# Kernel optimization log

Measured on AMD Instinct MI355X. Metric: run time of the kernel, lower is better.

Reference implementation:

```python
import jax, jax.numpy as jnp
import numpy as np

B, S, D, NH = 2, 2048, 2048, 16
HD = D // NH  # 128


def setup_inputs() -> dict:
    key = jax.random.key(0)
    ks = jax.random.split(key, 7)
    s = 1.0 / np.sqrt(D)
    return {
        "hidden_states": jax.random.normal(ks[0], (B, S, D), dtype=jnp.float32),
        "Wq": jax.random.normal(ks[1], (D, D), dtype=jnp.float32) * s,
        "Wk": jax.random.normal(ks[2], (D, D), dtype=jnp.float32) * s,
        "Wv": jax.random.normal(ks[3], (D, D), dtype=jnp.float32) * s,
        "Wo": jax.random.normal(ks[4], (D, D), dtype=jnp.float32) * s,
        # phase projections: hidden -> num_heads (zero-init in the module; use small
        # random values so the phase path is numerically exercised)
        "Wpq": jax.random.normal(ks[5], (D, NH), dtype=jnp.float32) * 0.02,
        "Wpk": jax.random.normal(ks[6], (D, NH), dtype=jnp.float32) * 0.02,
    }


def reference(hidden_states, Wq, Wk, Wv, Wo, Wpq, Wpk):
    x = hidden_states  # [B,S,D]
    # ---- base_attn: standard causal multi-head self-attention ----
    q = (x @ Wq).reshape(B, S, NH, HD).transpose(0, 2, 1, 3)  # [B,H,S,hd]
    k = (x @ Wk).reshape(B, S, NH, HD).transpose(0, 2, 1, 3)
    v = (x @ Wv).reshape(B, S, NH, HD).transpose(0, 2, 1, 3)
    scores = jnp.einsum("bhqd,bhkd->bhqk", q, k) / np.sqrt(HD)  # [B,H,S,S]
    causal = jnp.tril(jnp.ones((S, S), dtype=bool))
    scores = jnp.where(causal, scores, jnp.float32(-1e9))
    probs = jax.nn.softmax(scores, axis=-1)
    ctx = jnp.einsum("bhqk,bhkd->bhqd", probs, v)  # [B,H,S,hd]
    attn_output = ctx.transpose(0, 2, 1, 3).reshape(B, S, D) @ Wo  # [B,S,D]
    # ---- phase modulation ----
    # original: cos(pq[b,q,None,h] - pk[b,None,k,h]).mean(dims=(k,h))  -> [B,S]
    # identity: cos(a-b) = cos a * cos b + sin a * sin b lets us avoid the
    # [B,S,S,H] tensor; the math is identical.
    pq = x @ Wpq  # [B,S,H]
    pk = x @ Wpk  # [B,S,H]
    Ck = jnp.cos(pk).sum(axis=1)  # [B,H]
    Sk = jnp.sin(pk).sum(axis=1)  # [B,H]
    phase_mod = (jnp.cos(pq) * Ck[:, None, :] + jnp.sin(pq) * Sk[:, None, :]).sum(-1) / (S * NH)  # [B,S]
    return attn_output * (1.0 + 0.1 * phase_mod[..., None])
```

## Files before the change

### kernel.cpp

```cpp
#include <hip/hip_runtime.h>
#include <hip/hip_bf16.h>

typedef __attribute__((ext_vector_type(8))) short short8;
typedef __attribute__((ext_vector_type(4))) float f32x4;
typedef __attribute__((ext_vector_type(16))) float f32x16;
typedef __attribute__((ext_vector_type(4))) int i32x4;
typedef unsigned short u16;

#define S_LEN 2048
#define D_DIM 2048
#define NHEAD 16
#define HDIM 128
#define M_ROWS 4096

#define MFMA(a,b,c) __builtin_amdgcn_mfma_f32_16x16x32_bf16(a,b,c,0,0,0)
#define MFMA32(a,b,c) __builtin_amdgcn_mfma_f32_32x32x16_bf16(a,b,c,0,0,0)

__device__ __forceinline__ u16 f2bf(float f) {
  union { float f; unsigned u; } v; v.f = f;
  unsigned r = v.u + 0x7fffu + ((v.u >> 16) & 1u);
  return (u16)(r >> 16);
}

__device__ __forceinline__ void async16(void* lds, const void* g) {
  __builtin_amdgcn_global_load_lds(
      (const __attribute__((address_space(1))) unsigned*)g,
      (__attribute__((address_space(3))) unsigned*)lds, 16, 0, 0);
}

__device__ __forceinline__ unsigned cvtpk(float lo, float hi) {
  unsigned r;
  asm("v_cvt_pk_bf16_f32 %0, %1, %2" : "=v"(r) : "v"(lo), "v"(hi));
  return r;
}
__device__ __forceinline__ void plswap(unsigned& x, unsigned& y) {
  asm("v_permlane32_swap_b32 %0, %1" : "+v"(x), "+v"(y));
}

__global__ __launch_bounds__(256) void k_prep(const float* __restrict__ W0,
                                              const float* __restrict__ W1,
                                              const float* __restrict__ W2,
                                              const float* __restrict__ W3,
                                              u16* __restrict__ T0, u16* __restrict__ T1,
                                              u16* __restrict__ T2, u16* __restrict__ T3,
                                              const float* __restrict__ x,
                                              u16* __restrict__ xb) {
  const int z = blockIdx.z;
  if (z < 4) {
    __shared__ u16 tile[32][33];
    const float* W = (z == 0) ? W0 : (z == 1) ? W1 : (z == 2) ? W2 : W3;
    u16* Wt = (z == 0) ? T0 : (z == 1) ? T1 : (z == 2) ? T2 : T3;
    int n0 = blockIdx.x * 32, k0 = blockIdx.y * 32;
    int tx = threadIdx.x & 31, ty = threadIdx.x >> 5;
#pragma unroll
    for (int i = 0; i < 4; i++)
      tile[ty + i * 8][tx] = f2bf(W[(size_t)(k0 + ty + i * 8) * D_DIM + n0 + tx]);
    __syncthreads();
#pragma unroll
    for (int i = 0; i < 4; i++)
      Wt[(size_t)(n0 + ty + i * 8) * D_DIM + k0 + tx] = tile[tx][ty + i * 8];
  } else {
    const int row0 = (z - 4) * 2048 + blockIdx.y * 32;
    const int col0 = blockIdx.x * 32;
    const int r = threadIdx.x >> 3, c4 = threadIdx.x & 7;
    const float4 v = *reinterpret_cast<const float4*>(
        &x[(size_t)(row0 + r) * D_DIM + col0 + c4 * 4]);
    ushort4 o;
    o.x = f2bf(v.x); o.y = f2bf(v.y); o.z = f2bf(v.z); o.w = f2bf(v.w);
    *reinterpret_cast<ushort4*>(&xb[(size_t)(row0 + r) * D_DIM + col0 + c4 * 4]) = o;
  }
}

template <int MODE>
__device__ __forceinline__ void gemm_body(const u16* __restrict__ A,
                                          const u16* __restrict__ Bt,
                                          void* __restrict__ outp,
                                          u16* __restrict__ Vt,
                                          const float* __restrict__ fac,
                                          char* lds) {
  constexpr int BUFSZ = 49152;
  const int m0 = blockIdx.y * 128, n0 = blockIdx.x * 256;
  const int t = threadIdx.x;
  const int w = t >> 6, l = t & 63;
  const int wr = (w >> 2) * 64, wc = (w & 3) * 64;
  const int lr = l & 15, lq = l >> 4;
  const char* Ab = (const char*)A;
  const char* Bb = (const char*)Bt;

  f32x4 acc[4][4] = {};

  const int sub = w >> 2, ww = w & 3;
  const int abase = (ww & 1) * 16 + (ww >> 1) * 64;
  const int bbase = (w >> 1) * 64 + (w & 1) * 16;
  const int rr = l >> 2, sl = l & 3;

  auto stageA = [&](int tt, int nb, int mh) {
    const int base = abase + mh * 32;
    const int row = base + rr;
    async16(lds + nb * BUFSZ + sub * 8192 + base * 64,
            Ab + (size_t)(m0 + row) * 4096 + tt * 128 + sub * 64 +
                ((sl ^ ((row >> 1) & 3)) * 16));
  };
  auto stageB = [&](int tt, int nb, int nh) {
    const int base = bbase + nh * 32;
    const int row = base + rr;
#pragma unroll
    for (int j = 0; j < 2; j++)
      async16(lds + nb * BUFSZ + 16384 + j * 16384 + base * 64,
              Bb + (size_t)(n0 + row) * 4096 + tt * 128 + j * 64 +
                  ((sl ^ ((row >> 1) & 3)) * 16));
  };

  auto readA = [&](short8 af[2][2], int buf, int mh) {
#pragma unroll
    for (int mi = 0; mi < 2; mi++)
#pragma unroll
      for (int ks = 0; ks < 2; ks++) {
        const int row = wr + mh * 32 + mi * 16 + lr;
        af[mi][ks] = *reinterpret_cast<const short8*>(
            lds + buf * BUFSZ + ks * 8192 + row * 64 +
            ((lq ^ ((row >> 1) & 3)) * 16));
      }
  };
  auto readB = [&](short8 bf[2][2], int buf, int nh) {
#pragma unroll
    for (int ni = 0; ni < 2; ni++)
#pragma unroll
      for (int ks = 0; ks < 2; ks++) {
        const int row = wc + nh * 32 + ni * 16 + lr;
        bf[ni][ks] = *reinterpret_cast<const short8*>(
            lds + buf * BUFSZ + 16384 + ks * 16384 + row * 64 +
            ((lq ^ ((row >> 1) & 3)) * 16));
      }
  };

#define QUAD(AF, BF, MH, NH)                                                \
  {                                                                         \
    __builtin_amdgcn_s_setprio(1);                                          \
    _Pragma("unroll") for (int mi = 0; mi < 2; mi++)                        \
    _Pragma("unroll") for (int ni = 0; ni < 2; ni++)                        \
    _Pragma("unroll") for (int ks = 0; ks < 2; ks++)                        \
      acc[(MH)*2 + mi][(NH)*2 + ni] =                                       \
          MFMA(AF[mi][ks], BF[ni][ks], acc[(MH)*2 + mi][(NH)*2 + ni]);      \
    __builtin_amdgcn_s_setprio(0);                                          \
  }
#define VMW(N) asm volatile("s_waitcnt vmcnt(" #N ")" ::: "memory")
#define BAR()                         \
  do {                                \
    __builtin_amdgcn_s_barrier();     \
    asm volatile("" ::: "memory");    \
  } while (0)

  stageA(0, 0, 0); stageB(0, 0, 0);
  stageA(0, 0, 1);
  stageB(0, 0, 1);

  short8 af0[2][2], af1[2][2], bfr[2][2];
  const int NT = D_DIM / 64;
  for (int tt = 0; tt < NT; tt++) {
    const int buf = tt & 1, nb = buf ^ 1;
    const bool pf = (tt + 1 < NT);
    VMW(3); BAR();
    if (pf) { stageA(tt + 1, nb, 0); stageB(tt + 1, nb, 0); }
    readA(af0, buf, 0); readB(bfr, buf, 0);
    QUAD(af0, bfr, 0, 0);
    if (pf) VMW(5); else VMW(2);
    BAR();
    if (pf) stageA(tt + 1, nb, 1);
    readA(af1, buf, 1);
    QUAD(af1, bfr, 1, 0);
    if (pf) VMW(4); else VMW(0);
    BAR();
    if (pf) stageB(tt + 1, nb, 1);
    readB(bfr, buf, 1);
    QUAD(af1, bfr, 1, 1);
    BAR();
    QUAD(af0, bfr, 0, 1);
  }
#undef QUAD
#undef VMW
#undef BAR

#pragma unroll
  for (int gm = 0; gm < 4; gm++) {
#pragma unroll
    for (int gn = 0; gn < 4; gn++) {
      const int row0 = m0 + wr + gm * 16 + lq * 4;
      const int col = n0 + wc + gn * 16 + lr;
      if (MODE == 0) {
        if (col >= 4096) {
          const int d = col & 127, hh = (col >> 7) & 15;
          const int bb = row0 >> 11, s0 = row0 & 2047;
          ushort4 v4;
          v4.x = f2bf(acc[gm][gn][0]);
          v4.y = f2bf(acc[gm][gn][1]);
          v4.z = f2bf(acc[gm][gn][2]);
          v4.w = f2bf(acc[gm][gn][3]);
          *reinterpret_cast<ushort4*>(
              Vt + (((size_t)(bb * NHEAD + hh) * HDIM + d) * S_LEN + s0)) = v4;
        } else {
#pragma unroll
          for (int r = 0; r < 4; r++) {
            const int row = row0 + r;
            const int mat = col >> 11;
            const int hh = (col >> 7) & 15;
            ((u16*)outp)[(size_t)mat * 8388608 +
                         (((size_t)((row >> 11) * NHEAD + hh)) * S_LEN + (row & 2047)) * HDIM +
                         (col & 127)] = f2bf(acc[gm][gn][r]);
          }
        }
      } else {
#pragma unroll
        for (int r = 0; r < 4; r++) {
          const int row = row0 + r;
          ((float*)outp)[(size_t)row * D_DIM + col] =
              acc[gm][gn][r] * (1.0f + 0.1f * fac[row]);
        }
      }
    }
  }
}

__global__ __launch_bounds__(512, 1) void k_qkv(const u16* __restrict__ A,
                                                const u16* __restrict__ Bt,
                                                void* __restrict__ outp,
                                                u16* __restrict__ Vt) {
  __shared__ __align__(16) char lds[2 * 49152];
  gemm_body<0>(A, Bt, outp, Vt, nullptr, lds);
}

__global__ __launch_bounds__(512, 1) void k_oproj(const u16* __restrict__ A,
                                                  const u16* __restrict__ Bt,
                                                  void* __restrict__ outp,
                                                  const float* __restrict__ fac) {
  __shared__ __align__(16) char lds[2 * 49152];
  gemm_body<1>(A, Bt, outp, nullptr, fac, lds);
}

__global__ __launch_bounds__(256) void k_phase_proj(const u16* __restrict__ xb,
                                                    const float* __restrict__ Wpq,
                                                    const float* __restrict__ Wpk,
                                                    float* __restrict__ pq,
                                                    float* __restrict__ pk) {
  __shared__ u16 xs[16][136];
  __shared__ float2 ws[128][16];
  const int t = threadIdx.x;
  const int m0 = blockIdx.x * 16;
  const int h = t & 15, r = t >> 4;
  float sq = 0.f, sk = 0.f;
  for (int kc = 0; kc < D_DIM; kc += 128) {
    *reinterpret_cast<short8*>(&xs[t >> 4][(t & 15) * 8]) =
        *reinterpret_cast<const short8*>(
            &xb[(size_t)(m0 + (t >> 4)) * D_DIM + kc + (t & 15) * 8]);
#pragma unroll
    for (int j = 0; j < 8; j++) {
      const int idx = j * 256 + t;
      const int k = idx >> 4, hh = idx & 15;
      ws[k][hh] = make_float2(Wpq[(size_t)(kc + k) * NHEAD + hh],
                              Wpk[(size_t)(kc + k) * NHEAD + hh]);
    }
    __syncthreads();
#pragma unroll
    for (int k8 = 0; k8 < 16; k8++) {
      const short8 x8 = *reinterpret_cast<const short8*>(&xs[r][k8 * 8]);
#pragma unroll
      for (int j = 0; j < 8; j++) {
        union { float f; unsigned u; } c;
        c.u = ((unsigned)(u16)x8[j]) << 16;
        const float2 wv = ws[k8 * 8 + j][h];
        sq += c.f * wv.x;
        sk += c.f * wv.y;
      }
    }
    __syncthreads();
  }
  pq[(size_t)(m0 + r) * NHEAD + h] = sq;
  pk[(size_t)(m0 + r) * NHEAD + h] = sk;
}

__device__ __forceinline__ float wave_sum(float v) {
  v += __shfl_xor(v, 1);  v += __shfl_xor(v, 2);  v += __shfl_xor(v, 4);
  v += __shfl_xor(v, 8);  v += __shfl_xor(v, 16); v += __shfl_xor(v, 32);
  return v;
}

__global__ void k_phase_ck(const float* __restrict__ pk, float* __restrict__ Ck,
                           float* __restrict__ Sk) {
  int bh = blockIdx.x, b = bh >> 4, h = bh & 15;
  float c = 0.f, s = 0.f;
  for (int ss = threadIdx.x; ss < S_LEN; ss += 256) {
    float v = pk[((size_t)b * S_LEN + ss) * NHEAD + h];
    c += cosf(v); s += sinf(v);
  }
  c = wave_sum(c); s = wave_sum(s);
  __shared__ float rc[4], rs[4];
  int wv = threadIdx.x >> 6;
  if ((threadIdx.x & 63) == 0) { rc[wv] = c; rs[wv] = s; }
  __syncthreads();
  if (threadIdx.x == 0) {
    Ck[bh] = rc[0] + rc[1] + rc[2] + rc[3];
    Sk[bh] = rs[0] + rs[1] + rs[2] + rs[3];
  }
}

__global__ void k_phase_mod(const float* __restrict__ pq, const float* __restrict__ Ck,
                            const float* __restrict__ Sk, float* __restrict__ pm) {
  int m = blockIdx.x * 256 + threadIdx.x;
  int b = m >> 11;
  float a = 0.f;
#pragma unroll
  for (int h = 0; h < NHEAD; h++) {
    float v = pq[(size_t)m * NHEAD + h];
    a += cosf(v) * Ck[b * NHEAD + h] + sinf(v) * Sk[b * NHEAD + h];
  }
  pm[m] = a * (1.0f / (S_LEN * NHEAD));
}

__global__ __launch_bounds__(256, 2) void k_attn(const u16* __restrict__ Q,
                                                 const u16* __restrict__ K,
                                                 const u16* __restrict__ Vt,
                                                 u16* __restrict__ ctx) {
  const int bh = blockIdx.x;
  const int gy = blockIdx.y;
  const int g = (gy < 8) ? (15 - gy) : (gy - 8);
  const int b = bh >> 4, h = bh & 15;
  const int t = threadIdx.x;
  const int w = t >> 6, l = t & 63;
  const int ln = l & 31, hi = l >> 5;
  const int q0w = g * 128 + w * 32;
  const int qq = q0w + ln;
  const float sc2 = 0.08838834764831845f * 1.4426950408889634f;

  const u16* Qp = Q + (size_t)bh * S_LEN * HDIM;
  const char* Kg = (const char*)(K + (size_t)bh * S_LEN * HDIM);
  const char* Vg = (const char*)(Vt + (size_t)bh * HDIM * S_LEN);

  __shared__ __align__(16) char Ks[16384];
  __shared__ __align__(16) char Vs[16384];

  auto stage = [&](int t64) {
    const int k0 = t64 * 64;
#pragma unroll
    for (int i = 0; i < 4; i++) {
      const int key = i * 16 + w * 4 + (l >> 4);
      async16(Ks + i * 4096 + w * 1024,
              Kg + (size_t)(k0 + key) * 256 + (((l & 15) * 16) ^ ((key & 15) << 4)));
      const int d = i * 32 + w * 8 + (l >> 3);
      async16(Vs + i * 4096 + w * 1024,
              Vg + (size_t)d * (S_LEN * 2) + k0 * 2 + (((l & 7) * 16) ^ ((d & 7) << 4)));
    }
  };

  short8 qf[8];
#pragma unroll
  for (int c = 0; c < 8; c++)
    qf[c] = *reinterpret_cast<const short8*>(Qp + (size_t)qq * HDIM + c * 16 + hi * 8);

  f32x16 o[4];
#pragma unroll
  for (int ds = 0; ds < 4; ds++)
#pragma unroll
    for (int r = 0; r < 16; r++) o[ds][r] = 0.f;
  float mrun = -1e30f, lsum = 0.f;

  const int nt = (g + 1) * 2;
  for (int t64 = 0; t64 < nt; t64++) {
    const int k0 = t64 * 64;
    stage(t64);
    __syncthreads();
    if (k0 < q0w + 32) {
      f32x16 s[2];
#pragma unroll
      for (int ks = 0; ks < 2; ks++)
#pragma unroll
        for (int r = 0; r < 16; r++) s[ks][r] = 0.f;
      __builtin_amdgcn_s_setprio(1);
#pragma unroll
      for (int ks = 0; ks < 2; ks++) {
        const int key = ks * 32 + ln;
        const char* kb = Ks + key * 256;
        const unsigned swzk = (unsigned)((key & 15) << 4);
#pragma unroll
        for (int c = 0; c < 8; c++) {
          const short8 kf = *reinterpret_cast<const short8*>(
              kb + (((unsigned)(c * 32 + hi * 16)) ^ swzk));
          s[ks] = MFMA32(kf, qf[c], s[ks]);
        }
      }
      __builtin_amdgcn_s_setprio(0);
      float p[32];
      float mx = -1e30f;
      const bool interior = (k0 + 64 <= q0w + 1);
      if (interior) {
#pragma unroll
        for (int ks = 0; ks < 2; ks++)
#pragma unroll
          for (int r = 0; r < 16; r++) {
            const float v = s[ks][r] * sc2;
            p[ks * 16 + r] = v;
            mx = fmaxf(mx, v);
          }
      } else {
#pragma unroll
        for (int ks = 0; ks < 2; ks++)
#pragma unroll
          for (int r = 0; r < 16; r++) {
            const int key = k0 + ks * 32 + (r & 3) + 8 * (r >> 2) + 4 * hi;
            const float v = (key <= qq) ? s[ks][r] * sc2 : -1e30f;
            p[ks * 16 + r] = v;
            mx = fmaxf(mx, v);
          }
      }
      mx = fmaxf(mx, __shfl_xor(mx, 32));
      if (!__all(mx <= mrun + 11.0f)) {
        const float nm = fmaxf(mrun, mx);
        const float f = exp2f(mrun - nm);
        lsum *= f;
#pragma unroll
        for (int ds = 0; ds < 4; ds++)
#pragma unroll
          for (int r = 0; r < 16; r++) o[ds][r] *= f;
        mrun = nm;
      }
      float rs = 0.f;
#pragma unroll
      for (int i = 0; i < 32; i++) { p[i] = exp2f(p[i] - mrun); rs += p[i]; }
      rs += __shfl_xor(rs, 32);
      lsum += rs;
      short8 bfr[4];
#pragma unroll
      for (int sub = 0; sub < 2; sub++) {
#pragma unroll
        for (int half = 0; half < 2; half++) {
          const int pb = sub * 16 + half * 8;
          unsigned X1 = cvtpk(p[pb + 0], p[pb + 1]);
          unsigned X2 = cvtpk(p[pb + 2], p[pb + 3]);
          unsigned Y1 = cvtpk(p[pb + 4], p[pb + 5]);
          unsigned Y2 = cvtpk(p[pb + 6], p[pb + 7]);
          plswap(X1, Y1);
          plswap(X2, Y2);
          i32x4 bw;
          bw[0] = (int)X1; bw[1] = (int)X2; bw[2] = (int)Y1; bw[3] = (int)Y2;
          bfr[sub * 2 + half] = __builtin_bit_cast(short8, bw);
        }
      }
      __builtin_amdgcn_s_setprio(1);
#pragma unroll
      for (int ds = 0; ds < 4; ds++) {
        const int d = ds * 32 + ln;
        const char* vb = Vs + d * 128;
        const unsigned swzv = (unsigned)((d & 7) << 4);
#pragma unroll
        for (int slot = 0; slot < 4; slot++) {
          const short8 vf = *reinterpret_cast<const short8*>(
              vb + (((unsigned)(slot * 32 + hi * 16)) ^ swzv));
          o[ds] = MFMA32(vf, bfr[slot], o[ds]);
        }
      }
      __builtin_amdgcn_s_setprio(0);
    }
    __syncthreads();
  }

  const float rl = 1.0f / lsum;
#pragma unroll
  for (int ds = 0; ds < 4; ds++) {
#pragma unroll
    for (int rq = 0; rq < 4; rq++) {
      const int d = ds * 32 + 8 * rq + 4 * hi;
      ushort4 pk4;
      pk4.x = f2bf(o[ds][rq * 4 + 0] * rl);
      pk4.y = f2bf(o[ds][rq * 4 + 1] * rl);
      pk4.z = f2bf(o[ds][rq * 4 + 2] * rl);
      pk4.w = f2bf(o[ds][rq * 4 + 3] * rl);
      *reinterpret_cast<ushort4*>(ctx + ((size_t)(b * S_LEN + qq)) * D_DIM + h * HDIM + d) = pk4;
    }
  }
}

extern "C" void kernel_launch(void* const* d_in, const int* in_sizes, int n_in,
                              void* d_out, int out_size, void* d_ws, size_t ws_size,
                              hipStream_t stream) {
  const float* x   = (const float*)d_in[0];
  const float* Wq  = (const float*)d_in[1];
  const float* Wk  = (const float*)d_in[2];
  const float* Wv  = (const float*)d_in[3];
  const float* Wo  = (const float*)d_in[4];
  const float* Wpq = (const float*)d_in[5];
  const float* Wpk = (const float*)d_in[6];

  char* ws = (char*)d_ws;
  u16* xb   = (u16*)(ws + 0);
  u16* Wqt  = (u16*)(ws + 16777216);
  u16* Wkt  = (u16*)(ws + 25165824);
  u16* Wvt  = (u16*)(ws + 33554432);
  u16* Wot  = (u16*)(ws + 41943040);
  u16* Qb   = (u16*)(ws + 50331648);
  u16* Kb   = (u16*)(ws + 67108864);
  u16* Vb   = (u16*)(ws + 83886080);
  u16* Vt   = (u16*)(ws + 100663296);
  float* pq = (float*)(ws + 117440512);
  float* pk = (float*)(ws + 117702656);
  float* Ck = (float*)(ws + 117964800);
  float* Sk = (float*)(ws + 117964928);
  float* pm = (float*)(ws + 117965056);

  k_prep<<<dim3(64, 64, 6), 256, 0, stream>>>(Wq, Wk, Wv, Wo, Wqt, Wkt, Wvt, Wot, x, xb);

  k_qkv<<<dim3(24, 32), 512, 0, stream>>>(xb, Wqt, Qb, Vt);

  k_phase_proj<<<dim3(256), 256, 0, stream>>>(xb, Wpq, Wpk, pq, pk);
  k_phase_ck<<<dim3(32), 256, 0, stream>>>(pk, Ck, Sk);
  k_phase_mod<<<dim3(16), 256, 0, stream>>>(pq, Ck, Sk, pm);

  k_attn<<<dim3(32, 16), 256, 0, stream>>>(Qb, Kb, Vt, Vb );

  k_oproj<<<dim3(8, 32), 512, 0, stream>>>(Vb , Wot, (void*)d_out, pm);
}
```

Baseline: 322.0 us.

## Enlarge QKV GEMM block tile to 256x256 with dedicated kernel

The QKV projection gets its own kernel with a 256x256 output tile per block, up from 128x256. Each wave now accumulates 128x64, using 64 KB double-buffered LDS stages and interleaved async prefetch. Larger tiles raise arithmetic intensity and cut global reloads of A and B. In exchange, register pressure rises (128 accumulator floats per lane), the grid drops to 384 blocks, and LDS use grows to 128 KB. The O-projection keeps the old template body, specialised.

```diff
diff --git a/kernel.cpp b/kernel.cpp
--- a/kernel.cpp
+++ b/kernel.cpp
@@ -71,14 +71,147 @@
   }
 }
 
-template <int MODE>
-__device__ __forceinline__ void gemm_body(const u16* __restrict__ A,
-                                          const u16* __restrict__ Bt,
-                                          void* __restrict__ outp,
-                                          u16* __restrict__ Vt,
-                                          const float* __restrict__ fac,
-                                          char* lds) {
+__global__ __launch_bounds__(512, 1) void k_qkv(const u16* __restrict__ A,
+                                                const u16* __restrict__ Bt,
+                                                u16* __restrict__ outp,
+                                                u16* __restrict__ Vt) {
+  __shared__ __align__(16) char lds[131072];
+  const int m0 = blockIdx.y * 256, n0 = blockIdx.x * 256;
+  const int t = threadIdx.x;
+  const int w = t >> 6, l = t & 63;
+  const int wm = w >> 2, wn = w & 3, bn = wn >> 1;
+  const int wr = wm * 128, wc = wn * 64;
+  const int lr = l & 15, lq = l >> 4;
+  const char* Ab = (const char*)A;
+  const char* Bb = (const char*)Bt;
+
+  const int gia = wn;
+  const int gib = wm * 2 + (wn & 1);
+
+  f32x4 acc[8][4] = {};
+
+  auto stageA = [&](int tt, int nb, int jpair) {
+#pragma unroll
+    for (int jj = 0; jj < 2; jj++) {
+      const int s = jpair;
+      const int rblk = jj;
+      const int row = wm * 128 + rblk * 64 + gia * 16 + (l >> 2);
+      async16(lds + nb * 65536 + s * 16384 +
+                  (wm * 128 + rblk * 64 + gia * 16) * 64 + l * 16,
+              Ab + (size_t)(m0 + row) * 4096 + tt * 128 + s * 64 +
+                  (((l & 3) ^ ((row >> 1) & 3)) * 16));
+    }
+  };
+  auto stageB = [&](int tt, int nb, int jpair) {
+#pragma unroll
+    for (int jj = 0; jj < 2; jj++) {
+      const int s = jpair;
+      const int rblk = jj;
+      const int row = bn * 128 + rblk * 64 + gib * 16 + (l >> 2);
+      async16(lds + nb * 65536 + 32768 + s * 16384 +
+                  (bn * 128 + rblk * 64 + gib * 16) * 64 + l * 16,
+              Bb + (size_t)(n0 + row) * 4096 + tt * 128 + s * 64 +
+                  (((l & 3) ^ ((row >> 1) & 3)) * 16));
+    }
+  };
+
+  auto readA = [&](short8 af[4][2], int buf, int ms) {
+#pragma unroll
+    for (int mi = 0; mi < 4; mi++)
+#pragma unroll
+      for (int ks = 0; ks < 2; ks++) {
+        const int row = wr + ms * 64 + mi * 16 + lr;
+        af[mi][ks] = *reinterpret_cast<const short8*>(
+            lds + buf * 65536 + ks * 16384 + row * 64 +
+            ((lq ^ ((row >> 1) & 3)) * 16));
+      }
+  };
+  auto readB = [&](short8 bf[2][2], int buf, int ns) {
+#pragma unroll
+    for (int ni = 0; ni < 2; ni++)
+#pragma unroll
+      for (int ks = 0; ks < 2; ks++) {
+        const int row = wc + ns * 32 + ni * 16 + lr;
+        bf[ni][ks] = *reinterpret_cast<const short8*>(
+            lds + buf * 65536 + 32768 + ks * 16384 + row * 64 +
+            ((lq ^ ((row >> 1) & 3)) * 16));
+      }
+  };
+
+#define QUAD16(AF, BF, MS, NS)                                              \
+  {                                                                         \
+    __builtin_amdgcn_s_setprio(1);                                          \
+    _Pragma("unroll") for (int mi = 0; mi < 4; mi++)                        \
+    _Pragma("unroll") for (int ni = 0; ni < 2; ni++)                        \
+    _Pragma("unroll") for (int ks = 0; ks < 2; ks++)                        \
+      acc[(MS)*4 + mi][(NS)*2 + ni] =                                       \
+          MFMA(AF[mi][ks], BF[ni][ks], acc[(MS)*4 + mi][(NS)*2 + ni]);      \
+    __builtin_amdgcn_s_setprio(0);                                          \
+  }
+
+  stageA(0, 0, 0); stageA(0, 0, 1);
+  stageB(0, 0, 0); stageB(0, 0, 1);
+
+  short8 af0[4][2], af1[4][2], bf0[2][2], bf1[2][2];
+  const int NT = D_DIM / 64;
+  for (int tt = 0; tt < NT; tt++) {
+    const int buf = tt & 1, nb = buf ^ 1;
+    const bool pf = (tt + 1 < NT);
+    asm volatile("s_waitcnt lgkmcnt(0)" ::: "memory");
+    asm volatile("s_waitcnt vmcnt(0)" ::: "memory");
+    __builtin_amdgcn_s_barrier();
+    asm volatile("" ::: "memory");
+    if (pf) stageA(tt + 1, nb, 0);
+    readA(af0, buf, 0); readB(bf0, buf, 0);
+    QUAD16(af0, bf0, 0, 0);
+    if (pf) stageA(tt + 1, nb, 1);
+    readB(bf1, buf, 1);
+    QUAD16(af0, bf1, 0, 1);
+    if (pf) stageB(tt + 1, nb, 0);
+    readA(af1, buf, 1);
+    QUAD16(af1, bf1, 1, 1);
+    if (pf) stageB(tt + 1, nb, 1);
+    QUAD16(af1, bf0, 1, 0);
+  }
+#undef QUAD16
+
+#pragma unroll
+  for (int gm = 0; gm < 8; gm++) {
+#pragma unroll
+    for (int gn = 0; gn < 4; gn++) {
+      const int row0 = m0 + wr + gm * 16 + lq * 4;
+      const int col = n0 + wc + gn * 16 + lr;
+      if (col >= 4096) {
+        const int d = col & 127, hh = (col >> 7) & 15;
+        const int bb = row0 >> 11, s0 = row0 & 2047;
+        ushort4 v4;
+        v4.x = f2bf(acc[gm][gn][0]);
+        v4.y = f2bf(acc[gm][gn][1]);
+        v4.z = f2bf(acc[gm][gn][2]);
+        v4.w = f2bf(acc[gm][gn][3]);
+        *reinterpret_cast<ushort4*>(
+            Vt + (((size_t)(bb * NHEAD + hh) * HDIM + d) * S_LEN + s0)) = v4;
+      } else {
+#pragma unroll
+        for (int r = 0; r < 4; r++) {
+          const int row = row0 + r;
+          const int mat = col >> 11;
+          const int hh = (col >> 7) & 15;
+          outp[(size_t)mat * 8388608 +
+               (((size_t)((row >> 11) * NHEAD + hh)) * S_LEN + (row & 2047)) * HDIM +
+               (col & 127)] = f2bf(acc[gm][gn][r]);
+        }
+      }
+    }
+  }
+}
+
+__global__ __launch_bounds__(512, 1) void k_oproj(const u16* __restrict__ A,
+                                                  const u16* __restrict__ Bt,
+                                                  float* __restrict__ outp,
+                                                  const float* __restrict__ fac) {
   constexpr int BUFSZ = 49152;
+  __shared__ __align__(16) char lds[2 * 49152];
   const int m0 = blockIdx.y * 128, n0 = blockIdx.x * 256;
   const int t = threadIdx.x;
   const int w = t >> 6, l = t & 63;
@@ -110,7 +243,6 @@
               Bb + (size_t)(n0 + row) * 4096 + tt * 128 + j * 64 +
                   ((sl ^ ((row >> 1) & 3)) * 16));
   };
-
   auto readA = [&](short8 af[2][2], int buf, int mh) {
 #pragma unroll
     for (int mi = 0; mi < 2; mi++)
@@ -187,54 +319,14 @@
     for (int gn = 0; gn < 4; gn++) {
       const int row0 = m0 + wr + gm * 16 + lq * 4;
       const int col = n0 + wc + gn * 16 + lr;
-      if (MODE == 0) {
-        if (col >= 4096) {
-          const int d = col & 127, hh = (col >> 7) & 15;
-          const int bb = row0 >> 11, s0 = row0 & 2047;
-          ushort4 v4;
-          v4.x = f2bf(acc[gm][gn][0]);
-          v4.y = f2bf(acc[gm][gn][1]);
-          v4.z = f2bf(acc[gm][gn][2]);
-          v4.w = f2bf(acc[gm][gn][3]);
-          *reinterpret_cast<ushort4*>(
-              Vt + (((size_t)(bb * NHEAD + hh) * HDIM + d) * S_LEN + s0)) = v4;
-        } else {
-#pragma unroll
-          for (int r = 0; r < 4; r++) {
-            const int row = row0 + r;
-            const int mat = col >> 11;
-            const int hh = (col >> 7) & 15;
-            ((u16*)outp)[(size_t)mat * 8388608 +
-                         (((size_t)((row >> 11) * NHEAD + hh)) * S_LEN + (row & 2047)) * HDIM +
-                         (col & 127)] = f2bf(acc[gm][gn][r]);
-          }
-        }
-      } else {
-#pragma unroll
-        for (int r = 0; r < 4; r++) {
-          const int row = row0 + r;
-          ((float*)outp)[(size_t)row * D_DIM + col] =
-              acc[gm][gn][r] * (1.0f + 0.1f * fac[row]);
-        }
-      }
-    }
-  }
-}
-
-__global__ __launch_bounds__(512, 1) void k_qkv(const u16* __restrict__ A,
-                                                const u16* __restrict__ Bt,
-                                                void* __restrict__ outp,
-                                                u16* __restrict__ Vt) {
-  __shared__ __align__(16) char lds[2 * 49152];
-  gemm_body<0>(A, Bt, outp, Vt, nullptr, lds);
-}
-
-__global__ __launch_bounds__(512, 1) void k_oproj(const u16* __restrict__ A,
-                                                  const u16* __restrict__ Bt,
-                                                  void* __restrict__ outp,
-                                                  const float* __restrict__ fac) {
-  __shared__ __align__(16) char lds[2 * 49152];
-  gemm_body<1>(A, Bt, outp, nullptr, fac, lds);
+#pragma unroll
+      for (int r = 0; r < 4; r++) {
+        const int row = row0 + r;
+        outp[(size_t)row * D_DIM + col] =
+            acc[gm][gn][r] * (1.0f + 0.1f * fac[row]);
+      }
+    }
+  }
 }
 
 __global__ __launch_bounds__(256) void k_phase_proj(const u16* __restrict__ xb,
@@ -507,7 +599,7 @@
 
   k_prep<<<dim3(64, 64, 6), 256, 0, stream>>>(Wq, Wk, Wv, Wo, Wqt, Wkt, Wvt, Wot, x, xb);
 
-  k_qkv<<<dim3(24, 32), 512, 0, stream>>>(xb, Wqt, Qb, Vt);
+  k_qkv<<<dim3(24, 16), 512, 0, stream>>>(xb, Wqt, Qb, Vt);
 
   k_phase_proj<<<dim3(256), 256, 0, stream>>>(xb, Wpq, Wpk, pq, pk);
   k_phase_ck<<<dim3(32), 256, 0, stream>>>(pk, Ck, Sk);
@@ -515,5 +607,5 @@
 
   k_attn<<<dim3(32, 16), 256, 0, stream>>>(Qb, Kb, Vt, Vb );
 
-  k_oproj<<<dim3(8, 32), 512, 0, stream>>>(Vb , Wot, (void*)d_out, pm);
-}
+  k_oproj<<<dim3(8, 32), 512, 0, stream>>>(Vb , Wot, (float*)d_out, pm);
+}
```

Measured after the change: 327.0 us. Within noise of the previous version (+1.6%).
